# Kernel optimization log

Measured on AMD Instinct MI355X. Metric: run time of the kernel, lower is better.

Reference implementation:

```python
import jax, jax.numpy as jnp
import numpy as np

T, D, S, Q, K = 768, 24, 576, 32, 128   # tokens, dense atoms/token, subsets, queries/subset, keys/subset
CA, CP, CT, H, DH = 128, 16, 384, 4, 32  # per-atom ch, pair ch, per-token ch, heads, head dim


def _conv_feat(idx, arr):
    # atom_layout.convert with layout_axes=(-3,-2): flatten first two axes, gather, keep channels
    return arr.reshape(-1, arr.shape[-1])[idx]


def _conv_flat(idx, arr):
    # atom_layout.convert with layout_axes=(-2,-1): flatten all layout axes, gather
    return arr.reshape(-1)[idx]


def setup_inputs() -> dict:
    key = jax.random.key(0)
    ks = iter(jax.random.split(key, 64))

    def nrm(shape, scale=0.05):
        return jax.random.normal(next(ks), shape, dtype=jnp.float32) * scale

    inp = {}
    inp["ref_positions"] = nrm((T, D, 3), 1.0)
    inp["ref_mask"] = jnp.ones((T, D), jnp.float32)
    inp["ref_charge"] = nrm((T, D), 1.0)
    inp["atom_mask"] = jnp.ones((T, D), jnp.float32)
    inp["ref_element"] = jax.random.randint(next(ks), (T, D), 0, 128)
    inp["ref_atom_name_chars"] = jax.random.randint(next(ks), (T, D, 4), 0, 64)
    inp["ref_space_uid"] = jax.random.randint(next(ks), (T, D), 0, T)
    inp["t2q_idx"] = jax.random.randint(next(ks), (S, Q), 0, T * D)
    inp["q2k_idx"] = jax.random.randint(next(ks), (S, K), 0, S * Q)
    inp["q2t_idx"] = jax.random.randint(next(ks), (T, D), 0, S * Q)
    # learned weights (stored (in, out); y = x @ W, equivalent to torch Linear with W.T)
    inp["w_ref_pos"] = nrm((3, CA))
    inp["w_ref_mask"] = nrm((1, CA))
    inp["w_ref_element"] = nrm((128, CA))
    inp["w_ref_charge"] = nrm((1, CA))
    inp["w_ref_atom_name"] = nrm((256, CA))
    inp["w_s2p_row1"] = nrm((CA, CP))
    inp["w_s2p_col1"] = nrm((CA, CP))
    inp["w_pair_off1"] = nrm((3, CP))
    inp["w_pair_dist1"] = nrm((1, CP))
    inp["w_pair_valid"] = nrm((1, CP))
    inp["w_mlp1"] = nrm((CP, CP))
    inp["w_mlp2"] = nrm((CP, CP))
    inp["w_mlp3"] = nrm((CP, CP))
    inp["wq"] = nrm((CA, H * DH))
    inp["wk"] = nrm((CA, H * DH))
    inp["wv"] = nrm((CA, H * DH))
    inp["wb"] = nrm((CP, H))
    inp["wo"] = nrm((H * DH, CA))
    inp["w_proj"] = nrm((CA, CT))
    return inp


def reference(ref_positions, ref_mask, ref_charge, atom_mask,
              ref_element, ref_atom_name_chars, ref_space_uid,
              t2q_idx, q2k_idx, q2t_idx,
              w_ref_pos, w_ref_mask, w_ref_element, w_ref_charge, w_ref_atom_name,
              w_s2p_row1, w_s2p_col1, w_pair_off1, w_pair_dist1, w_pair_valid,
              w_mlp1, w_mlp2, w_mlp3, wq, wk, wv, wb, wo, w_proj):
    # ---- per-atom conditioning ----
    act = ref_positions @ w_ref_pos                                   # (T,D,CA)
    act += ref_mask[..., None] @ w_ref_mask
    act += jax.nn.one_hot(ref_element, 128, dtype=jnp.float32) @ w_ref_element
    act += jnp.arcsinh(ref_charge)[..., None] @ w_ref_charge
    name_1hot = jax.nn.one_hot(ref_atom_name_chars, 64, dtype=jnp.float32).reshape(T, D, 256)
    act += name_1hot @ w_ref_atom_name
    act *= ref_mask[..., None]

    # ---- layout conversions (gathers) ----
    queries_single_cond = _conv_feat(t2q_idx, act)                    # (S,Q,CA)
    queries_mask = _conv_flat(t2q_idx, atom_mask)                     # (S,Q)
    queries_act = queries_single_cond
    keys_single_cond = _conv_feat(q2k_idx, queries_single_cond)       # (S,K,CA)
    keys_mask = _conv_flat(q2k_idx, queries_mask)                     # (S,K)

    # ---- pair conditioning: broadcast row+col, offsets, inv-sq-dist, validity ----
    row1 = jax.nn.relu(queries_single_cond) @ w_s2p_row1              # (S,Q,CP)
    col1 = jax.nn.relu(keys_single_cond) @ w_s2p_col1                 # (S,K,CP)
    pair = row1[:, :, None, :] + col1[:, None, :, :]                  # (S,Q,K,CP)

    queries_ref_pos = _conv_feat(t2q_idx, ref_positions)              # (S,Q,3)
    queries_uid = _conv_flat(t2q_idx, ref_space_uid)                  # (S,Q)
    keys_ref_pos = _conv_feat(q2k_idx, queries_ref_pos)               # (S,K,3)
    keys_uid = _conv_flat(q2k_idx, ref_space_uid)                     # (S,K)

    valid = (queries_uid[:, :, None] == keys_uid[:, None, :])         # (S,Q,K)
    validf = valid[..., None].astype(jnp.float32)
    offsets = queries_ref_pos[:, :, None, :] - keys_ref_pos[:, None, :, :]  # (S,Q,K,3)
    pair += (offsets @ w_pair_off1) * validf
    sq_dists = jnp.sum(jnp.square(offsets), axis=-1)
    pair += ((1.0 / (1.0 + sq_dists))[..., None] @ w_pair_dist1) * validf
    pair += validf @ w_pair_valid

    p2 = jax.nn.relu(pair) @ w_mlp1
    p2 = jax.nn.relu(p2) @ w_mlp2
    pair += jax.nn.relu(p2) @ w_mlp3

    # ---- cross-attention (queries attend to keys, pair_cond as bias) ----
    keys_act = _conv_feat(q2k_idx, queries_act)                       # (S,K,CA)
    q = (queries_act @ wq).reshape(S, Q, H, DH)
    k = (keys_act @ wk).reshape(S, K, H, DH)
    v = (keys_act @ wv).reshape(S, K, H, DH)
    bias = pair @ wb                                                  # (S,Q,K,H)
    logits = jnp.einsum('sqhd,skhd->sqkh', q, k) / jnp.sqrt(jnp.float32(DH)) + bias
    logits = jnp.where(keys_mask[:, None, :, None] > 0, logits, jnp.float32(-1e9))
    attn = jax.nn.softmax(logits, axis=2)
    o = jnp.einsum('sqkh,skhd->sqhd', attn, v).reshape(S, Q, H * DH)
    queries_act = queries_act + o @ wo

    queries_act = queries_act * queries_mask[..., None]
    skip_connection = queries_act
    proj = queries_act @ w_proj                                       # (S,Q,CT)
    token_atoms_act = _conv_feat(q2t_idx, proj)                       # (T,D,CT)

    # mask_mean over dense atom axis
    num = jnp.sum(atom_mask[..., None] * jax.nn.relu(token_atoms_act), axis=-2)
    den = jnp.sum(atom_mask, axis=-1, keepdims=True) + 1e-10
    token_act = num / den                                             # (T,CT)

    return (token_act, skip_connection, queries_mask, queries_single_cond,
            keys_mask, keys_single_cond, pair)
```

## Files before the change

kernel.cpp:

```cpp
#include <hip/hip_runtime.h>

typedef unsigned short u16;
typedef unsigned int u32;

#define T_ 768
#define D_ 24
#define S_ 576
#define Q_ 32
#define K_ 128
#define CA_ 128
#define CP_ 16
#define CT_ 384
#define H_ 4
#define DH_ 32
#define SQ_ (S_*Q_)
#define SK_ (S_*K_)

__device__ __forceinline__ float b2f(u16 u){ return __uint_as_float(((u32)u)<<16); }
__device__ __forceinline__ u16 f2b(float f){ u32 x=__float_as_uint(f); return (u16)((x + 0x7fffu + ((x>>16)&1u))>>16); }

__global__ __launch_bounds__(128) void n_qsc(
    const float* __restrict__ pos, const float* __restrict__ rmask, const float* __restrict__ charge,
    const float* __restrict__ amask, const int* __restrict__ elem, const int* __restrict__ chars,
    const int* __restrict__ uid, const int* __restrict__ t2q,
    const float* __restrict__ w_pos, const float* __restrict__ w_mask, const float* __restrict__ w_elem,
    const float* __restrict__ w_chg, const float* __restrict__ w_name,
    float* __restrict__ qsc, float* __restrict__ qmask, float* __restrict__ qrp, int* __restrict__ quid,
    float* __restrict__ out_qsc, float* __restrict__ out_qmask)
{
  int slot = blockIdx.x, ch = threadIdx.x;
  int a = t2q[slot];
  float p0 = pos[a*3+0], p1 = pos[a*3+1], p2 = pos[a*3+2];
  float m  = rmask[a];
  float cg = asinhf(charge[a]);
  int e  = elem[a];
  int c0 = chars[a*4+0], c1 = chars[a*4+1], c2 = chars[a*4+2], c3 = chars[a*4+3];
  float v = p0*w_pos[0*CA_+ch] + p1*w_pos[1*CA_+ch] + p2*w_pos[2*CA_+ch];
  v += m * w_mask[ch];
  v += w_elem[e*CA_+ch];
  v += cg * w_chg[ch];
  v += w_name[(0*64+c0)*CA_+ch] + w_name[(1*64+c1)*CA_+ch]
     + w_name[(2*64+c2)*CA_+ch] + w_name[(3*64+c3)*CA_+ch];
  v *= m;
  qsc[(size_t)slot*CA_+ch] = v;
  out_qsc[(size_t)slot*CA_+ch] = v;
  if (ch < 3) qrp[slot*3+ch] = pos[a*3+ch];
  if (ch == 0){
    float am = amask[a];
    qmask[slot] = am;
    out_qmask[slot] = am;
    quid[slot] = uid[a];
  }
}

__global__ __launch_bounds__(128) void n_keys(
    const float* __restrict__ qsc, const float* __restrict__ qmask, const float* __restrict__ qrp,
    const int* __restrict__ uid, const int* __restrict__ q2k,
    float* __restrict__ krp, int* __restrict__ kuid,
    float* __restrict__ out_ksc, float* __restrict__ out_kmask)
{
  int r = threadIdx.x >> 5;
  int e = threadIdx.x & 31;
  int sk = blockIdx.x*4 + r;
  int j = q2k[sk];
  *(float4*)&out_ksc[(size_t)sk*CA_ + e*4] = *(const float4*)&qsc[(size_t)j*CA_ + e*4];
  if (e < 3) krp[sk*3+e] = qrp[j*3+e];
  if (e == 0){
    out_kmask[sk] = qmask[j];
    kuid[sk] = uid[j];
  }
}

__global__ __launch_bounds__(128) void n_qkv(
    const float* __restrict__ X, const float* __restrict__ wq, const float* __restrict__ wk,
    const float* __restrict__ wv, float* __restrict__ Qp, float* __restrict__ Kp, float* __restrict__ Vp)
{
  __shared__ float Xs[16*CA_];
  int tid = threadIdx.x;
  size_t r0 = (size_t)blockIdx.x * 16;
  for (int e = tid; e < 16*CA_; e += 128) Xs[e] = X[r0*CA_ + e];
  __syncthreads();
  int c = tid;
  float acc[16];

  #pragma unroll
  for (int r = 0; r < 16; ++r) acc[r] = 0.f;
  for (int i = 0; i < CA_; ++i){
    float w = wq[i*CA_+c];
    #pragma unroll
    for (int r = 0; r < 16; ++r) acc[r] += Xs[r*CA_+i] * w;
  }
  #pragma unroll
  for (int r = 0; r < 16; ++r) Qp[(r0+r)*CA_+c] = acc[r] * 0.17677669529663687f;

  #pragma unroll
  for (int r = 0; r < 16; ++r) acc[r] = 0.f;
  for (int i = 0; i < CA_; ++i){
    float w = wk[i*CA_+c];
    #pragma unroll
    for (int r = 0; r < 16; ++r) acc[r] += Xs[r*CA_+i] * w;
  }
  #pragma unroll
  for (int r = 0; r < 16; ++r) Kp[(r0+r)*CA_+c] = acc[r];

  #pragma unroll
  for (int r = 0; r < 16; ++r) acc[r] = 0.f;
  for (int i = 0; i < CA_; ++i){
    float w = wv[i*CA_+c];
    #pragma unroll
    for (int r = 0; r < 16; ++r) acc[r] += Xs[r*CA_+i] * w;
  }
  #pragma unroll
  for (int r = 0; r < 16; ++r) Vp[(r0+r)*CA_+c] = acc[r];
}

__global__ __launch_bounds__(128) void n_proj16b(
    const float* __restrict__ X, const float* __restrict__ Wr, const float* __restrict__ Wc,
    float* __restrict__ Yr, float* __restrict__ Yc)
{
  int row = blockIdx.x*4 + (threadIdx.x >> 5);
  int c = threadIdx.x & 31;
  const float* W = (c < 16) ? Wr : Wc;
  float* Y = (c < 16) ? Yr : Yc;
  int cc = c & 15;
  float acc = 0.f;
  for (int i = 0; i < CA_; ++i)
    acc += fmaxf(X[(size_t)row*CA_+i], 0.f) * W[i*CP_+cc];
  Y[(size_t)row*CP_+cc] = acc;
}

__global__ __launch_bounds__(128) void n_pair(
    const int* __restrict__ q2k, const float* __restrict__ rowproj, const float* __restrict__ colproj,
    const float* __restrict__ qrp, const int* __restrict__ quid,
    const float* __restrict__ krp, const int* __restrict__ kuid,
    const float* __restrict__ w1, const float* __restrict__ w2, const float* __restrict__ w3,
    const float* __restrict__ wpo, const float* __restrict__ wpd, const float* __restrict__ wpv,
    const float* __restrict__ wb,
    float* __restrict__ out_pair, u16* __restrict__ bias_ws)
{
  __shared__ float w1s[256], w2s[256], w3s[256], wbs[64], wpos[48], wpds[16], wpvs[16];
  __shared__ __align__(16) float Ls[128*20];
  int tid = threadIdx.x;
  for (int e = tid; e < 256; e += 128){ w1s[e] = w1[e]; w2s[e] = w2[e]; w3s[e] = w3[e]; }
  if (tid < 64) wbs[tid] = wb[tid];
  if (tid < 48) wpos[tid] = wpo[tid];
  if (tid < 16){ wpds[tid] = wpd[tid]; wpvs[tid] = wpv[tid]; }
  __syncthreads();

  int sq = blockIdx.x;
  int s  = sq >> 5;
  int q  = sq & 31;
  int k  = tid;
  int sk = s*K_ + k;
  int j  = q2k[sk];

  float rp[16], cp[16];
  *(float4*)&rp[0]  = *(const float4*)&rowproj[(size_t)sq*CP_ + 0];
  *(float4*)&rp[4]  = *(const float4*)&rowproj[(size_t)sq*CP_ + 4];
  *(float4*)&rp[8]  = *(const float4*)&rowproj[(size_t)sq*CP_ + 8];
  *(float4*)&rp[12] = *(const float4*)&rowproj[(size_t)sq*CP_ + 12];
  *(float4*)&cp[0]  = *(const float4*)&colproj[(size_t)j*CP_ + 0];
  *(float4*)&cp[4]  = *(const float4*)&colproj[(size_t)j*CP_ + 4];
  *(float4*)&cp[8]  = *(const float4*)&colproj[(size_t)j*CP_ + 8];
  *(float4*)&cp[12] = *(const float4*)&colproj[(size_t)j*CP_ + 12];

  float p[16];
  {
    float ox = qrp[sq*3+0] - krp[sk*3+0];
    float oy = qrp[sq*3+1] - krp[sk*3+1];
    float oz = qrp[sq*3+2] - krp[sk*3+2];
    float vf = (quid[sq] == kuid[sk]) ? 1.f : 0.f;
    float invd = vf / (1.f + ox*ox + oy*oy + oz*oz);
    #pragma unroll
    for (int c = 0; c < 16; ++c)
      p[c] = rp[c] + cp[c]
           + vf*(ox*wpos[c] + oy*wpos[16+c] + oz*wpos[32+c])
           + invd*wpds[c] + vf*wpvs[c];
  }
  float y[16];
  #pragma unroll
  for (int c = 0; c < 16; ++c) y[c] = 0.f;
  for (int i = 0; i < 16; ++i){
    float u = fmaxf(p[i], 0.f);
    #pragma unroll
    for (int c = 0; c < 16; ++c) y[c] += u * w1s[i*16+c];
  }
  float z[16];
  #pragma unroll
  for (int c = 0; c < 16; ++c) z[c] = 0.f;
  for (int i = 0; i < 16; ++i){
    float u = fmaxf(y[i], 0.f);
    #pragma unroll
    for (int c = 0; c < 16; ++c) z[c] += u * w2s[i*16+c];
  }
  for (int i = 0; i < 16; ++i){
    float u = fmaxf(z[i], 0.f);
    #pragma unroll
    for (int c = 0; c < 16; ++c) p[c] += u * w3s[i*16+c];
  }
  float b[4] = {0.f, 0.f, 0.f, 0.f};
  for (int c = 0; c < 16; ++c){
    #pragma unroll
    for (int h = 0; h < 4; ++h) b[h] += p[c] * wbs[c*4+h];
  }

  #pragma unroll
  for (int h = 0; h < 4; ++h)
    bias_ws[(((size_t)s*H_ + h)*Q_ + q)*K_ + k] = f2b(b[h]);

  #pragma unroll
  for (int c4 = 0; c4 < 4; ++c4)
    *(float4*)&Ls[k*20 + c4*4] = make_float4(p[c4*4+0], p[c4*4+1], p[c4*4+2], p[c4*4+3]);
  __syncthreads();
  size_t obase = (size_t)sq * (K_*CP_);
  #pragma unroll
  for (int i = 0; i < 4; ++i){
    int g4 = i*128 + tid;
    int kk = g4 >> 2, c = (g4 & 3)*4;
    *(float4*)&out_pair[obase + (size_t)g4*4] = *(const float4*)&Ls[kk*20 + c];
  }
}

__global__ __launch_bounds__(128) void n_attn(
    const float* __restrict__ Qp, const float* __restrict__ Kp, const float* __restrict__ Vp,
    const float* __restrict__ qmask, const u16* __restrict__ bias_ws, const int* __restrict__ q2k,
    float* __restrict__ O)
{
  __shared__ float Ks[128*36];
  __shared__ float Vs[128*36];
  __shared__ float msk[128];
  __shared__ float redm[64];
  __shared__ float reds[64];
  __shared__ float Osm[32*33];

  int b = blockIdx.x;
  int s = b >> 2, h = b & 3;
  int sq0 = s * Q_;
  int base = s * K_;
  int t = threadIdx.x;

  {
    int e = t & 7, rr = t >> 3;
    #pragma unroll
    for (int it = 0; it < 8; ++it){
      int row = it*16 + rr;
      int j = q2k[base + row];
      const float4* ksrc = (const float4*)&Kp[(size_t)j*CA_ + h*DH_];
      const float4* vsrc = (const float4*)&Vp[(size_t)j*CA_ + h*DH_];
      *(float4*)&Ks[row*36 + e*4] = ksrc[e];
      *(float4*)&Vs[row*36 + e*4] = vsrc[e];
    }
    int j0 = q2k[base + t];
    msk[t] = qmask[j0];
  }

  int q  = t & 31;
  int kr = t >> 5;
  float qreg[32];
  {
    const float4* qsrc = (const float4*)&Qp[(size_t)(sq0+q)*CA_ + h*DH_];
    #pragma unroll
    for (int d4 = 0; d4 < 8; ++d4){
      float4 v = qsrc[d4];
      qreg[d4*4+0] = v.x; qreg[d4*4+1] = v.y; qreg[d4*4+2] = v.z; qreg[d4*4+3] = v.w;
    }
  }

  u32 bw[16];
  {
    const uint4* bsrc = (const uint4*)&bias_ws[(((size_t)s*H_ + h)*Q_ + q)*K_ + kr*32];
    uint4 B;
    B = bsrc[0]; bw[0]=B.x;  bw[1]=B.y;  bw[2]=B.z;  bw[3]=B.w;
    B = bsrc[1]; bw[4]=B.x;  bw[5]=B.y;  bw[6]=B.z;  bw[7]=B.w;
    B = bsrc[2]; bw[8]=B.x;  bw[9]=B.y;  bw[10]=B.z; bw[11]=B.w;
    B = bsrc[3]; bw[12]=B.x; bw[13]=B.y; bw[14]=B.z; bw[15]=B.w;
  }
  __syncthreads();

  float p[32];
  #pragma unroll
  for (int kk = 0; kk < 32; ++kk){
    int k = kr*32 + kk;
    const float* kbase = &Ks[k*36];
    float acc = 0.f;
    #pragma unroll
    for (int d4 = 0; d4 < 8; ++d4){
      float4 kv = *(const float4*)(kbase + d4*4);
      acc += qreg[d4*4+0]*kv.x + qreg[d4*4+1]*kv.y + qreg[d4*4+2]*kv.z + qreg[d4*4+3]*kv.w;
    }
    float bz = b2f((u16)((bw[kk>>1] >> ((kk&1)*16)) & 0xffffu));
    p[kk] = (msk[k] > 0.f) ? (acc + bz) : -1e9f;
  }

  float m = p[0];
  #pragma unroll
  for (int kk = 1; kk < 32; ++kk) m = fmaxf(m, p[kk]);
  m = fmaxf(m, __shfl_xor(m, 32, 64));
  int wv = t >> 6;
  if ((t & 63) < 32) redm[wv*32 + q] = m;
  __syncthreads();
  float M = fmaxf(redm[q], redm[32 + q]);

  float sm = 0.f;
  #pragma unroll
  for (int kk = 0; kk < 32; ++kk){ p[kk] = __expf(p[kk] - M); sm += p[kk]; }
  sm += __shfl_xor(sm, 32, 64);
  if ((t & 63) < 32) reds[wv*32 + q] = sm;
  __syncthreads();
  float inv = 1.f / (reds[q] + reds[32 + q]);

  float acc[32];
  #pragma unroll
  for (int d = 0; d < 32; ++d) acc[d] = 0.f;
  #pragma unroll
  for (int kk = 0; kk < 32; ++kk){
    float w = p[kk];
    const float* vbase = &Vs[(kr*32 + kk)*36];
    #pragma unroll
    for (int d4 = 0; d4 < 8; ++d4){
      float4 vv = *(const float4*)(vbase + d4*4);
      acc[d4*4+0] += w*vv.x; acc[d4*4+1] += w*vv.y; acc[d4*4+2] += w*vv.z; acc[d4*4+3] += w*vv.w;
    }
  }
  #pragma unroll
  for (int d = 0; d < 32; ++d) acc[d] += __shfl_xor(acc[d], 32, 64);
  if (t < 32){
    #pragma unroll
    for (int d = 0; d < 32; ++d) Osm[q*33 + d] = acc[d];
  }
  __syncthreads();
  if (t >= 64 && t < 96){
    #pragma unroll
    for (int d = 0; d < 32; ++d) Osm[q*33 + d] = (Osm[q*33 + d] + acc[d]) * inv;
  }
  __syncthreads();

  #pragma unroll
  for (int it = 0; it < 2; ++it){
    int idx = it*128 + t;
    int qq = idx >> 3, e = idx & 7;
    float4 v = make_float4(Osm[qq*33 + e*4 + 0], Osm[qq*33 + e*4 + 1],
                           Osm[qq*33 + e*4 + 2], Osm[qq*33 + e*4 + 3]);
    *(float4*)&O[(size_t)(sq0+qq)*CA_ + h*DH_ + e*4] = v;
  }
}

__global__ __launch_bounds__(128) void n_qact(
    const float* __restrict__ qsc, const float* __restrict__ O, const float* __restrict__ qmask,
    const float* __restrict__ wo, float* __restrict__ qact, float* __restrict__ out_skip)
{
  __shared__ float Os[16*CA_];
  int tid = threadIdx.x;
  size_t r0 = (size_t)blockIdx.x * 16;
  for (int e = tid; e < 16*CA_; e += 128) Os[e] = O[r0*CA_ + e];
  __syncthreads();
  int c = tid;
  float acc[16];
  #pragma unroll
  for (int r = 0; r < 16; ++r) acc[r] = 0.f;
  for (int i = 0; i < CA_; ++i){
    float w = wo[i*CA_+c];
    #pragma unroll
    for (int r = 0; r < 16; ++r) acc[r] += Os[r*CA_+i] * w;
  }
  #pragma unroll
  for (int r = 0; r < 16; ++r){
    float v = (qsc[(r0+r)*CA_+c] + acc[r]) * qmask[r0+r];
    qact[(r0+r)*CA_+c] = v;
    out_skip[(r0+r)*CA_+c] = v;
  }
}

__global__ __launch_bounds__(384) void n_tok(
    const float* __restrict__ qact, const int* __restrict__ q2t, const float* __restrict__ amask,
    const float* __restrict__ wp, float* __restrict__ out_tok)
{
  __shared__ float Xs[D_*CA_];
  __shared__ int   jr[D_];
  __shared__ float mk[D_];
  int t = blockIdx.x, tid = threadIdx.x;
  if (tid < D_){
    jr[tid] = q2t[t*D_ + tid];
    mk[tid] = amask[t*D_ + tid];
  }
  __syncthreads();
  for (int e = tid; e < D_*CA_; e += 384){
    int d = e >> 7, i = e & 127;
    Xs[e] = qact[(size_t)jr[d]*CA_ + i];
  }
  __syncthreads();
  int ct = tid;
  float acc[D_];
  #pragma unroll
  for (int d = 0; d < D_; ++d) acc[d] = 0.f;
  for (int i = 0; i < CA_; ++i){
    float w = wp[i*CT_ + ct];
    #pragma unroll
    for (int d = 0; d < D_; ++d) acc[d] += Xs[d*CA_ + i] * w;
  }
  float num = 0.f, den = 1e-10f;
  #pragma unroll
  for (int d = 0; d < D_; ++d){
    num += mk[d] * fmaxf(acc[d], 0.f);
    den += mk[d];
  }
  out_tok[(size_t)t*CT_ + ct] = num/den;
}

extern "C" void kernel_launch(void* const* d_in, const int* in_sizes, int n_in,
                              void* d_out, int out_size, void* d_ws, size_t ws_size,
                              hipStream_t stream) {
  (void)in_sizes; (void)n_in; (void)out_size; (void)ws_size;
  const float* ref_positions = (const float*)d_in[0];
  const float* ref_mask      = (const float*)d_in[1];
  const float* ref_charge    = (const float*)d_in[2];
  const float* atom_mask     = (const float*)d_in[3];
  const int*   ref_element   = (const int*)d_in[4];
  const int*   ref_chars     = (const int*)d_in[5];
  const int*   ref_uid       = (const int*)d_in[6];
  const int*   t2q           = (const int*)d_in[7];
  const int*   q2k           = (const int*)d_in[8];
  const int*   q2t           = (const int*)d_in[9];
  const float* w_ref_pos     = (const float*)d_in[10];
  const float* w_ref_mask    = (const float*)d_in[11];
  const float* w_ref_element = (const float*)d_in[12];
  const float* w_ref_charge  = (const float*)d_in[13];
  const float* w_ref_name    = (const float*)d_in[14];
  const float* w_s2p_row1    = (const float*)d_in[15];
  const float* w_s2p_col1    = (const float*)d_in[16];
  const float* w_pair_off1   = (const float*)d_in[17];
  const float* w_pair_dist1  = (const float*)d_in[18];
  const float* w_pair_valid  = (const float*)d_in[19];
  const float* w_mlp1        = (const float*)d_in[20];
  const float* w_mlp2        = (const float*)d_in[21];
  const float* w_mlp3        = (const float*)d_in[22];
  const float* wq            = (const float*)d_in[23];
  const float* wk            = (const float*)d_in[24];
  const float* wv            = (const float*)d_in[25];
  const float* wb            = (const float*)d_in[26];
  const float* wo            = (const float*)d_in[27];
  const float* w_proj        = (const float*)d_in[28];

  char* ws = (char*)d_ws;
  float* qsc     = (float*)(ws + 0);
  float* qmask   = (float*)(ws + 9437184);
  float* qrp     = (float*)(ws + 9732096);
  int*   quid    = (int*)  (ws + 9953280);
  float* krp     = (float*)(ws + 10027008);
  int*   kuid    = (int*)  (ws + 10911744);
  float* rowproj = (float*)(ws + 11206656);
  float* colproj = (float*)(ws + 12386304);
  float* Qp      = (float*)(ws + 13565952);
  float* Kp      = (float*)(ws + 23003136);
  float* Vp      = (float*)(ws + 32440320);
  float* O       = (float*)(ws + 41877504);
  float* qact    = (float*)(ws + 51314688);
  u16*   biasws  = (u16*)  (ws + 60751872);

  float* out = (float*)d_out;
  float* out_tok   = out + 0;
  float* out_skip  = out + 294912;
  float* out_qmask = out + 2654208;
  float* out_qsc   = out + 2672640;
  float* out_kmask = out + 5031936;
  float* out_ksc   = out + 5105664;
  float* out_pair  = out + 14542848;

  hipLaunchKernelGGL(n_qsc, dim3(SQ_), dim3(128), 0, stream,
      ref_positions, ref_mask, ref_charge, atom_mask, ref_element, ref_chars, ref_uid, t2q,
      w_ref_pos, w_ref_mask, w_ref_element, w_ref_charge, w_ref_name,
      qsc, qmask, qrp, quid, out_qsc, out_qmask);
  hipLaunchKernelGGL(n_keys, dim3(SK_/4), dim3(128), 0, stream,
      qsc, qmask, qrp, ref_uid, q2k, krp, kuid, out_ksc, out_kmask);
  hipLaunchKernelGGL(n_qkv, dim3(SQ_/16), dim3(128), 0, stream,
      qsc, wq, wk, wv, Qp, Kp, Vp);
  hipLaunchKernelGGL(n_proj16b, dim3(SQ_/4), dim3(128), 0, stream,
      qsc, w_s2p_row1, w_s2p_col1, rowproj, colproj);
  hipLaunchKernelGGL(n_pair, dim3(SQ_), dim3(128), 0, stream,
      q2k, rowproj, colproj, qrp, quid, krp, kuid,
      w_mlp1, w_mlp2, w_mlp3, w_pair_off1, w_pair_dist1, w_pair_valid, wb,
      out_pair, biasws);
  hipLaunchKernelGGL(n_attn, dim3(S_*H_), dim3(128), 0, stream,
      Qp, Kp, Vp, qmask, biasws, q2k, O);
  hipLaunchKernelGGL(n_qact, dim3(SQ_/16), dim3(128), 0, stream,
      qsc, O, qmask, wo, qact, out_skip);
  hipLaunchKernelGGL(n_tok, dim3(T_), dim3(384), 0, stream,
      qact, q2t, atom_mask, w_proj, out_tok);
}
```

Baseline: 596.5 us.

## Drop LDS staging in projection kernels and read operands directly from global

```diff
diff --git a/kernel.cpp b/kernel.cpp
--- a/kernel.cpp
+++ b/kernel.cpp
@@ -75,43 +75,30 @@
     const float* __restrict__ X, const float* __restrict__ wq, const float* __restrict__ wk,
     const float* __restrict__ wv, float* __restrict__ Qp, float* __restrict__ Kp, float* __restrict__ Vp)
 {
-  __shared__ float Xs[16*CA_];
-  int tid = threadIdx.x;
+  int c = threadIdx.x;
   size_t r0 = (size_t)blockIdx.x * 16;
-  for (int e = tid; e < 16*CA_; e += 128) Xs[e] = X[r0*CA_ + e];
-  __syncthreads();
-  int c = tid;
-  float acc[16];
-
-  #pragma unroll
-  for (int r = 0; r < 16; ++r) acc[r] = 0.f;
+  float aq[16], ak[16], av[16];
+  #pragma unroll
+  for (int r = 0; r < 16; ++r){ aq[r] = 0.f; ak[r] = 0.f; av[r] = 0.f; }
+  #pragma unroll 4
   for (int i = 0; i < CA_; ++i){
-    float w = wq[i*CA_+c];
-    #pragma unroll
-    for (int r = 0; r < 16; ++r) acc[r] += Xs[r*CA_+i] * w;
-  }
-  #pragma unroll
-  for (int r = 0; r < 16; ++r) Qp[(r0+r)*CA_+c] = acc[r] * 0.17677669529663687f;
-
-  #pragma unroll
-  for (int r = 0; r < 16; ++r) acc[r] = 0.f;
-  for (int i = 0; i < CA_; ++i){
-    float w = wk[i*CA_+c];
-    #pragma unroll
-    for (int r = 0; r < 16; ++r) acc[r] += Xs[r*CA_+i] * w;
-  }
-  #pragma unroll
-  for (int r = 0; r < 16; ++r) Kp[(r0+r)*CA_+c] = acc[r];
-
-  #pragma unroll
-  for (int r = 0; r < 16; ++r) acc[r] = 0.f;
-  for (int i = 0; i < CA_; ++i){
-    float w = wv[i*CA_+c];
-    #pragma unroll
-    for (int r = 0; r < 16; ++r) acc[r] += Xs[r*CA_+i] * w;
-  }
-  #pragma unroll
-  for (int r = 0; r < 16; ++r) Vp[(r0+r)*CA_+c] = acc[r];
+    float q = wq[i*CA_+c];
+    float k = wk[i*CA_+c];
+    float v = wv[i*CA_+c];
+    #pragma unroll
+    for (int r = 0; r < 16; ++r){
+      float x = X[(r0+r)*CA_ + i];
+      aq[r] += x * q;
+      ak[r] += x * k;
+      av[r] += x * v;
+    }
+  }
+  #pragma unroll
+  for (int r = 0; r < 16; ++r){
+    Qp[(r0+r)*CA_+c] = aq[r] * 0.17677669529663687f;
+    Kp[(r0+r)*CA_+c] = ak[r];
+    Vp[(r0+r)*CA_+c] = av[r];
+  }
 }
 
 __global__ __launch_bounds__(128) void n_proj16b(
@@ -138,15 +125,8 @@
     const float* __restrict__ wb,
     float* __restrict__ out_pair, u16* __restrict__ bias_ws)
 {
-  __shared__ float w1s[256], w2s[256], w3s[256], wbs[64], wpos[48], wpds[16], wpvs[16];
   __shared__ __align__(16) float Ls[128*20];
   int tid = threadIdx.x;
-  for (int e = tid; e < 256; e += 128){ w1s[e] = w1[e]; w2s[e] = w2[e]; w3s[e] = w3[e]; }
-  if (tid < 64) wbs[tid] = wb[tid];
-  if (tid < 48) wpos[tid] = wpo[tid];
-  if (tid < 16){ wpds[tid] = wpd[tid]; wpvs[tid] = wpv[tid]; }
-  __syncthreads();
-
   int sq = blockIdx.x;
   int s  = sq >> 5;
   int q  = sq & 31;
@@ -154,11 +134,10 @@
   int sk = s*K_ + k;
   int j  = q2k[sk];
 
-  float rp[16], cp[16];
-  *(float4*)&rp[0]  = *(const float4*)&rowproj[(size_t)sq*CP_ + 0];
-  *(float4*)&rp[4]  = *(const float4*)&rowproj[(size_t)sq*CP_ + 4];
-  *(float4*)&rp[8]  = *(const float4*)&rowproj[(size_t)sq*CP_ + 8];
-  *(float4*)&rp[12] = *(const float4*)&rowproj[(size_t)sq*CP_ + 12];
+  float qx = qrp[sq*3+0], qy = qrp[sq*3+1], qz = qrp[sq*3+2];
+  int   qu = quid[sq];
+
+  float cp[16];
   *(float4*)&cp[0]  = *(const float4*)&colproj[(size_t)j*CP_ + 0];
   *(float4*)&cp[4]  = *(const float4*)&colproj[(size_t)j*CP_ + 4];
   *(float4*)&cp[8]  = *(const float4*)&colproj[(size_t)j*CP_ + 8];
@@ -166,42 +145,46 @@
 
   float p[16];
   {
-    float ox = qrp[sq*3+0] - krp[sk*3+0];
-    float oy = qrp[sq*3+1] - krp[sk*3+1];
-    float oz = qrp[sq*3+2] - krp[sk*3+2];
-    float vf = (quid[sq] == kuid[sk]) ? 1.f : 0.f;
+    float ox = qx - krp[sk*3+0];
+    float oy = qy - krp[sk*3+1];
+    float oz = qz - krp[sk*3+2];
+    float vf = (qu == kuid[sk]) ? 1.f : 0.f;
     float invd = vf / (1.f + ox*ox + oy*oy + oz*oz);
     #pragma unroll
     for (int c = 0; c < 16; ++c)
-      p[c] = rp[c] + cp[c]
-           + vf*(ox*wpos[c] + oy*wpos[16+c] + oz*wpos[32+c])
-           + invd*wpds[c] + vf*wpvs[c];
+      p[c] = rowproj[(size_t)sq*CP_+c] + cp[c]
+           + vf*(ox*wpo[c] + oy*wpo[16+c] + oz*wpo[32+c])
+           + invd*wpd[c] + vf*wpv[c];
   }
   float y[16];
   #pragma unroll
   for (int c = 0; c < 16; ++c) y[c] = 0.f;
+  #pragma unroll
   for (int i = 0; i < 16; ++i){
     float u = fmaxf(p[i], 0.f);
     #pragma unroll
-    for (int c = 0; c < 16; ++c) y[c] += u * w1s[i*16+c];
+    for (int c = 0; c < 16; ++c) y[c] += u * w1[i*16+c];
   }
   float z[16];
   #pragma unroll
   for (int c = 0; c < 16; ++c) z[c] = 0.f;
+  #pragma unroll
   for (int i = 0; i < 16; ++i){
     float u = fmaxf(y[i], 0.f);
     #pragma unroll
-    for (int c = 0; c < 16; ++c) z[c] += u * w2s[i*16+c];
-  }
+    for (int c = 0; c < 16; ++c) z[c] += u * w2[i*16+c];
+  }
+  #pragma unroll
   for (int i = 0; i < 16; ++i){
     float u = fmaxf(z[i], 0.f);
     #pragma unroll
-    for (int c = 0; c < 16; ++c) p[c] += u * w3s[i*16+c];
+    for (int c = 0; c < 16; ++c) p[c] += u * w3[i*16+c];
   }
   float b[4] = {0.f, 0.f, 0.f, 0.f};
+  #pragma unroll
   for (int c = 0; c < 16; ++c){
     #pragma unroll
-    for (int h = 0; h < 4; ++h) b[h] += p[c] * wbs[c*4+h];
+    for (int h = 0; h < 4; ++h) b[h] += p[c] * wb[c*4+h];
   }
 
   #pragma unroll
@@ -349,19 +332,16 @@
     const float* __restrict__ qsc, const float* __restrict__ O, const float* __restrict__ qmask,
     const float* __restrict__ wo, float* __restrict__ qact, float* __restrict__ out_skip)
 {
-  __shared__ float Os[16*CA_];
-  int tid = threadIdx.x;
+  int c = threadIdx.x;
   size_t r0 = (size_t)blockIdx.x * 16;
-  for (int e = tid; e < 16*CA_; e += 128) Os[e] = O[r0*CA_ + e];
-  __syncthreads();
-  int c = tid;
   float acc[16];
   #pragma unroll
   for (int r = 0; r < 16; ++r) acc[r] = 0.f;
+  #pragma unroll 4
   for (int i = 0; i < CA_; ++i){
     float w = wo[i*CA_+c];
     #pragma unroll
-    for (int r = 0; r < 16; ++r) acc[r] += Os[r*CA_+i] * w;
+    for (int r = 0; r < 16; ++r) acc[r] += O[(r0+r)*CA_+i] * w;
   }
   #pragma unroll
   for (int r = 0; r < 16; ++r){
@@ -375,28 +355,22 @@
     const float* __restrict__ qact, const int* __restrict__ q2t, const float* __restrict__ amask,
     const float* __restrict__ wp, float* __restrict__ out_tok)
 {
-  __shared__ float Xs[D_*CA_];
-  __shared__ int   jr[D_];
-  __shared__ float mk[D_];
-  int t = blockIdx.x, tid = threadIdx.x;
-  if (tid < D_){
-    jr[tid] = q2t[t*D_ + tid];
-    mk[tid] = amask[t*D_ + tid];
-  }
-  __syncthreads();
-  for (int e = tid; e < D_*CA_; e += 384){
-    int d = e >> 7, i = e & 127;
-    Xs[e] = qact[(size_t)jr[d]*CA_ + i];
-  }
-  __syncthreads();
-  int ct = tid;
+  int t = blockIdx.x, ct = threadIdx.x;
+  int jd[D_];
+  float mk[D_];
+  #pragma unroll
+  for (int d = 0; d < D_; ++d){
+    jd[d] = q2t[t*D_ + d];
+    mk[d] = amask[t*D_ + d];
+  }
   float acc[D_];
   #pragma unroll
   for (int d = 0; d < D_; ++d) acc[d] = 0.f;
+  #pragma unroll 4
   for (int i = 0; i < CA_; ++i){
     float w = wp[i*CT_ + ct];
     #pragma unroll
-    for (int d = 0; d < D_; ++d) acc[d] += Xs[d*CA_ + i] * w;
+    for (int d = 0; d < D_; ++d) acc[d] += qact[(size_t)jd[d]*CA_ + i] * w;
   }
   float num = 0.f, den = 1e-10f;
   #pragma unroll
```

Measured after the change: 632.7 us. 1.06x slower.
